# Kernel tuning notes

Hardware: AMD Instinct MI355X
Metric: run time of the kernel (lower is better)

## Reference

```python
import jax, jax.numpy as jnp
import numpy as np

N_CELLS = 50000
N_GENES = 2000
HIDDEN = 128
HEADS = 4
HEAD_DIM = HIDDEN // HEADS
E_FULL = 800000
E_PRUNED = 400000
LN_EPS = 1e-6
NEG_SLOPE = 0.2


def setup_inputs() -> dict:
    key = jax.random.key(0)
    ks = jax.random.split(key, 20)
    s_in = 1.0 / np.sqrt(N_GENES)
    s_h = 1.0 / np.sqrt(HIDDEN)
    inp = {
        "node_features": jax.random.normal(ks[0], (N_CELLS, N_GENES), jnp.float32),
        "full_edge_index": jax.random.randint(ks[1], (2, E_FULL), 0, N_CELLS, jnp.int64 if jax.config.jax_enable_x64 else jnp.int32),
        "full_edge_weights": jax.random.uniform(ks[2], (E_FULL, 1), jnp.float32),
        "pruned_edge_index": jax.random.randint(ks[3], (2, E_PRUNED), 0, N_CELLS, jnp.int64 if jax.config.jax_enable_x64 else jnp.int32),
        "pruned_edge_weights": jax.random.uniform(ks[4], (E_PRUNED, 1), jnp.float32),
        "alpha": jax.random.uniform(ks[5], (), jnp.float32),
        # input projection
        "ip_w": jax.random.normal(ks[6], (N_GENES, HIDDEN), jnp.float32) * s_in,
        "ip_b": jnp.zeros((HIDDEN,), jnp.float32),
        # GAT full graph
        "gf_wsrc": jax.random.normal(ks[7], (HIDDEN, HIDDEN), jnp.float32) * s_h,
        "gf_wdst": jax.random.normal(ks[8], (HIDDEN, HIDDEN), jnp.float32) * s_h,
        "gf_wedge": jax.random.normal(ks[9], (1, HIDDEN), jnp.float32),
        "gf_attn": jax.random.normal(ks[10], (HEADS, HEAD_DIM), jnp.float32) * (1.0 / np.sqrt(HEAD_DIM)),
        "gf_bias": jnp.zeros((HIDDEN,), jnp.float32),
        # GAT pruned graph
        "gp_wsrc": jax.random.normal(ks[11], (HIDDEN, HIDDEN), jnp.float32) * s_h,
        "gp_wdst": jax.random.normal(ks[12], (HIDDEN, HIDDEN), jnp.float32) * s_h,
        "gp_wedge": jax.random.normal(ks[13], (1, HIDDEN), jnp.float32),
        "gp_attn": jax.random.normal(ks[14], (HEADS, HEAD_DIM), jnp.float32) * (1.0 / np.sqrt(HEAD_DIM)),
        "gp_bias": jnp.zeros((HIDDEN,), jnp.float32),
        # LayerNorm
        "ln_scale": jnp.ones((HIDDEN,), jnp.float32),
        "ln_bias": jnp.zeros((HIDDEN,), jnp.float32),
    }
    return inp


def _gatv2(h, edge_index, edge_w, wsrc, wdst, wedge, attn, bias):
    """GATv2 with edge features: e_ij = a_h . leaky_relu(Ws h_i + Wd h_j + We w_ij),
    segment-softmax over destination nodes, scatter-aggregate Ws h_src, concat heads."""
    n = h.shape[0]
    src, dst = edge_index[0], edge_index[1]
    hs = (h @ wsrc).reshape(n, HEADS, HEAD_DIM)
    hd = (h @ wdst).reshape(n, HEADS, HEAD_DIM)
    ew = (edge_w @ wedge).reshape(-1, HEADS, HEAD_DIM)  # [E,H,D]
    z = jax.nn.leaky_relu(hs[src] + hd[dst] + ew, NEG_SLOPE)  # [E,H,D]
    logits = jnp.einsum('ehd,hd->eh', z, attn)  # [E,H]
    # segment softmax over incoming edges of each dst node
    m = jax.ops.segment_max(logits, dst, num_segments=n)
    m = jnp.where(jnp.isfinite(m), m, 0.0)
    ex = jnp.exp(logits - m[dst])
    denom = jax.ops.segment_sum(ex, dst, num_segments=n)
    att = ex / (denom[dst] + 1e-16)  # [E,H]
    out = jax.ops.segment_sum(att[..., None] * hs[src], dst, num_segments=n)  # [n,H,D]
    return out.reshape(n, HIDDEN) + bias


def _layer_norm(x, scale, bias):
    mu = jnp.mean(x, axis=-1, keepdims=True)
    var = jnp.mean(jnp.square(x - mu), axis=-1, keepdims=True)
    return (x - mu) * jax.lax.rsqrt(var + LN_EPS) * scale + bias


def reference(node_features, full_edge_index, full_edge_weights, pruned_edge_index,
              pruned_edge_weights, alpha, ip_w, ip_b,
              gf_wsrc, gf_wdst, gf_wedge, gf_attn, gf_bias,
              gp_wsrc, gp_wdst, gp_wedge, gp_attn, gp_bias,
              ln_scale, ln_bias):
    h = node_features @ ip_w + ip_b  # [n, hidden]
    h_full = _gatv2(h, full_edge_index, full_edge_weights, gf_wsrc, gf_wdst, gf_wedge, gf_attn, gf_bias)
    h_pruned = _gatv2(h, pruned_edge_index, pruned_edge_weights, gp_wsrc, gp_wdst, gp_wedge, gp_attn, gp_bias)
    h = (1.0 - alpha) * h_full + alpha * h_pruned
    h = jax.nn.elu(h)
    return _layer_norm(h, ln_scale, ln_bias)
```

## Files before the change

### kernel.cpp

```cpp
#include <hip/hip_runtime.h>
#include <hip/hip_bf16.h>

#define N_GENES 2000
#define SA 72
#define SH 136

typedef __attribute__((ext_vector_type(8))) short frag8;
typedef __attribute__((ext_vector_type(4))) float facc4;

static __device__ __forceinline__ unsigned short f2bf(float f) {
    unsigned int u = __float_as_uint(f);
    unsigned int r = (u + 0x7FFFu + ((u >> 16) & 1u)) >> 16;
    return (unsigned short)r;
}
static __device__ __forceinline__ ushort2 pk2(float a, float b) {
    __hip_bfloat162 r = __float22bfloat162_rn(float2{a, b});
    return *(ushort2*)&r;
}

__global__ void prep(const float* __restrict__ ip_w,
                     const float* __restrict__ ws_f, const float* __restrict__ wd_f,
                     const float* __restrict__ ws_p, const float* __restrict__ wd_p,
                     unsigned short* __restrict__ Bt1,
                     unsigned short* __restrict__ Bf, unsigned short* __restrict__ Bp,
                     int* __restrict__ deg, unsigned int* __restrict__ counter, int n2) {
    int idx = blockIdx.x * blockDim.x + threadIdx.x;
    if (idx < n2) deg[idx] = 0;
    if (idx == 0) counter[0] = 0u;
    if (idx < 128 * 2048) {
        int nrow = idx >> 11, k = idx & 2047;
        unsigned short v = 0;
        if (k < N_GENES) v = f2bf(ip_w[(size_t)k * 128 + nrow]);
        Bt1[idx] = v;
    } else {
        int q = idx - 128 * 2048;
        if (q >= 2 * 256 * 128) return;
        int g = q >> 15;
        int r = (q >> 7) & 255;
        int k = q & 127;
        const float* w = (g == 0) ? (r < 128 ? ws_f : wd_f) : (r < 128 ? ws_p : wd_p);
        (g == 0 ? Bf : Bp)[(r << 7) | k] = f2bf(w[k * 128 + (r & 127)]);
    }
}

__global__ __launch_bounds__(256) void gemm_deg(const float* __restrict__ A,
                                                const unsigned short* __restrict__ Bt,
                                                const float* __restrict__ bias,
                                                const unsigned short* __restrict__ Bf,
                                                const unsigned short* __restrict__ Bp,
                                                unsigned short* __restrict__ Cf,
                                                unsigned short* __restrict__ Cp,
                                                int M, int K, int gemmBlocks,
                                                const int* __restrict__ dst_f, int Ef,
                                                const int* __restrict__ dst_p, int Ep,
                                                int* __restrict__ deg, int N) {
    if (blockIdx.x >= gemmBlocks) {
        int e = (blockIdx.x - gemmBlocks) * 256 + threadIdx.x;
        if (e < Ef) atomicAdd(&deg[dst_f[e]], 1);
        else if (e < Ef + Ep) atomicAdd(&deg[N + dst_p[e - Ef]], 1);
        return;
    }
    const int Kpad = 2048;
    __shared__ __align__(16) unsigned short lA[64 * SA];
    __shared__ __align__(16) unsigned short lH[64 * SH];
    int t = threadIdx.x, lane = t & 63, wv = t >> 6;
    int lr = lane & 15, lq = lane >> 4;
    facc4 acc[4][2];
#pragma unroll
    for (int i = 0; i < 4; i++)
#pragma unroll
        for (int j = 0; j < 2; j++) acc[i][j] = (facc4){0.f, 0.f, 0.f, 0.f};
    int row_base = blockIdx.x * 64;

    int ar_r[4], ar_c[4];
    const float* ar_p[4];
#pragma unroll
    for (int j = 0; j < 4; j++) {
        int q = j * 256 + t;
        ar_r[j] = q >> 4;
        ar_c[j] = (q & 15) * 4;
        int rg = row_base + ar_r[j];
        if (rg >= M) rg = M - 1;
        ar_p[j] = A + (size_t)rg * K + ar_c[j];
    }
    const unsigned short* bp[4];
#pragma unroll
    for (int ks = 0; ks < 2; ks++)
#pragma unroll
        for (int ni = 0; ni < 2; ni++) {
            int col = wv * 32 + ni * 16 + lr;
            bp[ks * 2 + ni] = Bt + (size_t)col * Kpad + ks * 32 + lq * 8;
        }

    float4 ar[4];
    frag8 bfr[4];
#pragma unroll
    for (int j = 0; j < 4; j++) ar[j] = *(const float4*)(ar_p[j]);
#pragma unroll
    for (int f = 0; f < 4; f++) bfr[f] = *(const frag8*)(bp[f]);

    for (int k0 = 0; k0 < Kpad; k0 += 64) {
        __syncthreads();
#pragma unroll
        for (int j = 0; j < 4; j++) {
            ushort2 u01 = pk2(ar[j].x, ar[j].y);
            ushort2 u23 = pk2(ar[j].z, ar[j].w);
            ushort4 u = {u01.x, u01.y, u23.x, u23.y};
            *(ushort4*)&lA[ar_r[j] * SA + ar_c[j]] = u;
        }
        __syncthreads();
        int kn = k0 + 64;
        frag8 bfn[4];
        if (kn < Kpad) {
#pragma unroll
            for (int j = 0; j < 4; j++) {
                int kk = kn + ar_c[j];
                float4 v = {0.f, 0.f, 0.f, 0.f};
                if (kk < K) v = *(const float4*)(ar_p[j] + kn);
                ar[j] = v;
            }
#pragma unroll
            for (int f = 0; f < 4; f++) bfn[f] = *(const frag8*)(bp[f] + kn);
        }
#pragma unroll
        for (int ks = 0; ks < 2; ks++) {
            frag8 af[4];
#pragma unroll
            for (int mi = 0; mi < 4; mi++)
                af[mi] = *(const frag8*)&lA[(mi * 16 + lr) * SA + ks * 32 + lq * 8];
#pragma unroll
            for (int mi = 0; mi < 4; mi++)
#pragma unroll
                for (int ni = 0; ni < 2; ni++)
                    acc[mi][ni] = __builtin_amdgcn_mfma_f32_16x16x32_bf16(af[mi], bfr[ks * 2 + ni], acc[mi][ni], 0, 0, 0);
        }
        if (kn < Kpad) {
#pragma unroll
            for (int f = 0; f < 4; f++) bfr[f] = bfn[f];
        }
    }
    __syncthreads();
#pragma unroll
    for (int mi = 0; mi < 4; mi++) {
#pragma unroll
        for (int r = 0; r < 4; r++) {
            int row = mi * 16 + lq * 4 + r;
#pragma unroll
            for (int ni = 0; ni < 2; ni++) {
                int col = wv * 32 + ni * 16 + lr;
                lH[row * SH + col] = f2bf(acc[mi][ni][r] + bias[col]);
            }
        }
    }
    __syncthreads();
#pragma unroll 1
    for (int g = 0; g < 2; g++) {
        const unsigned short* B2 = g ? Bp : Bf;
        unsigned short* Cb = g ? Cp : Cf;
        facc4 a2[4][4];
#pragma unroll
        for (int i = 0; i < 4; i++)
#pragma unroll
            for (int j = 0; j < 4; j++) a2[i][j] = (facc4){0.f, 0.f, 0.f, 0.f};
#pragma unroll
        for (int ks = 0; ks < 4; ks++) {
            frag8 af[4], bf[4];
#pragma unroll
            for (int mi = 0; mi < 4; mi++)
                af[mi] = *(const frag8*)&lH[(mi * 16 + lr) * SH + ks * 32 + lq * 8];
#pragma unroll
            for (int ni = 0; ni < 4; ni++)
                bf[ni] = *(const frag8*)(B2 + ((wv * 64 + ni * 16 + lr) << 7) + ks * 32 + lq * 8);
#pragma unroll
            for (int mi = 0; mi < 4; mi++)
#pragma unroll
                for (int ni = 0; ni < 4; ni++)
                    a2[mi][ni] = __builtin_amdgcn_mfma_f32_16x16x32_bf16(af[mi], bf[ni], a2[mi][ni], 0, 0, 0);
        }
#pragma unroll
        for (int mi = 0; mi < 4; mi++) {
#pragma unroll
            for (int r = 0; r < 4; r++) {
                int row = row_base + mi * 16 + lq * 4 + r;
                if (row < M) {
#pragma unroll
                    for (int ni = 0; ni < 4; ni++) {
                        int col = wv * 64 + ni * 16 + lr;
                        Cb[(size_t)row * 256 + col] = f2bf(a2[mi][ni][r]);
                    }
                }
            }
        }
    }
}

__global__ __launch_bounds__(256) void seg_assign(const int* __restrict__ deg,
                                                  int* __restrict__ offs,
                                                  int* __restrict__ cur,
                                                  unsigned int* __restrict__ counter, int n2) {
    __shared__ int wbase[4];
    int t = threadIdx.x;
    int i = blockIdx.x * 256 + t;
    int lane = t & 63, wv = t >> 6;
    int c = (i < n2) ? deg[i] : 0;
    int incl = c;
#pragma unroll
    for (int o = 1; o < 64; o <<= 1) {
        int y = __shfl_up(incl, o);
        if (lane >= o) incl += y;
    }
    if (lane == 63) wbase[wv] = incl;
    __syncthreads();
    if (t == 0) {
        int s0 = wbase[0], s1 = wbase[1], s2 = wbase[2], s3 = wbase[3];
        int b = (int)atomicAdd(counter, (unsigned int)(s0 + s1 + s2 + s3));
        wbase[0] = b;
        wbase[1] = b + s0;
        wbase[2] = b + s0 + s1;
        wbase[3] = b + s0 + s1 + s2;
    }
    __syncthreads();
    int start = wbase[wv] + incl - c;
    if (i < n2) { offs[i] = start; cur[i] = start; }
}

__global__ void fill2(const int* __restrict__ src_f, const int* __restrict__ dst_f,
                      const float* __restrict__ ew_f, int Ef,
                      const int* __restrict__ src_p, const int* __restrict__ dst_p,
                      const float* __restrict__ ew_p, int Ep,
                      int* __restrict__ cur, int2* __restrict__ srcw, int N) {
    int e = blockIdx.x * blockDim.x + threadIdx.x;
    if (e >= Ef + Ep) return;
    int g = (e >= Ef);
    int ee = g ? e - Ef : e;
    int d = g ? dst_p[ee] : dst_f[ee];
    int node = g ? N + d : d;
    int p = atomicAdd(&cur[node], 1);
    int s = g ? src_p[ee] : src_f[ee];
    float w = g ? ew_p[ee] : ew_f[ee];
    srcw[p] = make_int2(s, __float_as_int(w));
}

__global__ __launch_bounds__(256) void gat2(const int* __restrict__ offs,
                                            const int* __restrict__ deg,
                                            const int2* __restrict__ srcw,
                                            const unsigned short* __restrict__ hshd_f,
                                            const unsigned short* __restrict__ hshd_p,
                                            const float* __restrict__ wedge_f,
                                            const float* __restrict__ attn_f,
                                            const float* __restrict__ bias_f,
                                            const float* __restrict__ wedge_p,
                                            const float* __restrict__ attn_p,
                                            const float* __restrict__ bias_p,
                                            float* __restrict__ out_full,
                                            float* __restrict__ out_pruned, int N) {
    int wid = blockIdx.x * 4 + (threadIdx.x >> 6);
    if (wid * 2 >= 2 * N) return;
    int lane = threadIdx.x & 63;
    int half = lane >> 5;
    int wl = lane & 31;
    int node = wid * 2 + half;
    int g = node >= N;
    int onode = g ? node - N : node;
    const unsigned short* hshd = g ? hshd_p : hshd_f;
    const float* wedge = g ? wedge_p : wedge_f;
    const float* attn = g ? attn_p : attn_f;
    const float* bias = g ? bias_p : bias_f;
    float* out = g ? out_pruned : out_full;
    int d4 = wl * 4;
    const float LOG2E = 1.4426950408889634f;
    float4 wv4 = *(const float4*)&wedge[d4];
    float4 av4 = *(const float4*)&attn[d4];
    av4.x *= LOG2E; av4.y *= LOG2E; av4.z *= LOG2E; av4.w *= LOG2E;
    uint2 hdr = *(const uint2*)&hshd[(size_t)onode * 256 + 128 + d4];
    const float hd0 = __uint_as_float(hdr.x << 16);
    const float hd1 = __uint_as_float(hdr.x & 0xffff0000u);
    const float hd2 = __uint_as_float(hdr.y << 16);
    const float hd3 = __uint_as_float(hdr.y & 0xffff0000u);
    int s = offs[node], cnt = deg[node];
    if (cnt <= 0) s = 0;
    int mc = max(cnt, __shfl_xor(cnt, 32));
    float m = -INFINITY, l = 0.f;
    float a0 = 0.f, a1 = 0.f, a2 = 0.f, a3 = 0.f;
    if (mc > 0) {
        int last = s + (cnt > 0 ? cnt : 1) - 1;
        auto CL = [last](int j) { return j > last ? last : j; };
        int2 e0 = srcw[CL(s)], e1 = srcw[CL(s + 1)], e2 = srcw[CL(s + 2)], e3 = srcw[CL(s + 3)];
        int2 e4 = srcw[CL(s + 4)], e5 = srcw[CL(s + 5)];
        uint2 hr0 = *(const uint2*)&hshd[(size_t)e0.x * 256 + d4];
        uint2 hr1 = *(const uint2*)&hshd[(size_t)e1.x * 256 + d4];
        uint2 hr2 = *(const uint2*)&hshd[(size_t)e2.x * 256 + d4];
        uint2 hr3 = *(const uint2*)&hshd[(size_t)e3.x * 256 + d4];
        for (int i = 0; i < mc; i += 2) {
            int2 ea = srcw[CL(s + i + 6)], eb = srcw[CL(s + i + 7)];
            uint2 hr4 = *(const uint2*)&hshd[(size_t)e4.x * 256 + d4];
            uint2 hr5 = *(const uint2*)&hshd[(size_t)e5.x * 256 + d4];
            {
                float h0 = __uint_as_float(hr0.x << 16);
                float h1 = __uint_as_float(hr0.x & 0xffff0000u);
                float h2 = __uint_as_float(hr0.y << 16);
                float h3 = __uint_as_float(hr0.y & 0xffff0000u);
                float w = __int_as_float(e0.y);
                float z0 = fmaf(w, wv4.x, h0 + hd0); z0 = (z0 > 0.f) ? z0 : 0.2f * z0;
                float z1 = fmaf(w, wv4.y, h1 + hd1); z1 = (z1 > 0.f) ? z1 : 0.2f * z1;
                float z2 = fmaf(w, wv4.z, h2 + hd2); z2 = (z2 > 0.f) ? z2 : 0.2f * z2;
                float z3 = fmaf(w, wv4.w, h3 + hd3); z3 = (z3 > 0.f) ? z3 : 0.2f * z3;
                float t = fmaf(z3, av4.w, fmaf(z2, av4.z, fmaf(z1, av4.y, z0 * av4.x)));
                t += __shfl_xor(t, 1);
                t += __shfl_xor(t, 2);
                t += __shfl_xor(t, 4);
                float mn = fmaxf(m, t);
                float sc = __builtin_amdgcn_exp2f(m - mn);
                float p = __builtin_amdgcn_exp2f(t - mn);
                p = (i < cnt) ? p : 0.f;
                l = l * sc + p;
                a0 = fmaf(p, h0, a0 * sc);
                a1 = fmaf(p, h1, a1 * sc);
                a2 = fmaf(p, h2, a2 * sc);
                a3 = fmaf(p, h3, a3 * sc);
                m = mn;
            }
            {
                float h0 = __uint_as_float(hr1.x << 16);
                float h1 = __uint_as_float(hr1.x & 0xffff0000u);
                float h2 = __uint_as_float(hr1.y << 16);
                float h3 = __uint_as_float(hr1.y & 0xffff0000u);
                float w = __int_as_float(e1.y);
                float z0 = fmaf(w, wv4.x, h0 + hd0); z0 = (z0 > 0.f) ? z0 : 0.2f * z0;
                float z1 = fmaf(w, wv4.y, h1 + hd1); z1 = (z1 > 0.f) ? z1 : 0.2f * z1;
                float z2 = fmaf(w, wv4.z, h2 + hd2); z2 = (z2 > 0.f) ? z2 : 0.2f * z2;
                float z3 = fmaf(w, wv4.w, h3 + hd3); z3 = (z3 > 0.f) ? z3 : 0.2f * z3;
                float t = fmaf(z3, av4.w, fmaf(z2, av4.z, fmaf(z1, av4.y, z0 * av4.x)));
                t += __shfl_xor(t, 1);
                t += __shfl_xor(t, 2);
                t += __shfl_xor(t, 4);
                float mn = fmaxf(m, t);
                float sc = __builtin_amdgcn_exp2f(m - mn);
                float p = __builtin_amdgcn_exp2f(t - mn);
                p = (i + 1 < cnt) ? p : 0.f;
                l = l * sc + p;
                a0 = fmaf(p, h0, a0 * sc);
                a1 = fmaf(p, h1, a1 * sc);
                a2 = fmaf(p, h2, a2 * sc);
                a3 = fmaf(p, h3, a3 * sc);
                m = mn;
            }
            e0 = e2; e1 = e3; e2 = e4; e3 = e5; e4 = ea; e5 = eb;
            hr0 = hr2; hr1 = hr3; hr2 = hr4; hr3 = hr5;
        }
    }
    float inv = 1.f / (l + 1e-16f);
    const float4 bv = *(const float4*)&bias[d4];
    float4 o;
    o.x = fmaf(a0, inv, bv.x);
    o.y = fmaf(a1, inv, bv.y);
    o.z = fmaf(a2, inv, bv.z);
    o.w = fmaf(a3, inv, bv.w);
    *(float4*)&out[(size_t)onode * 128 + d4] = o;
}

__global__ __launch_bounds__(256) void final_kernel(const float* __restrict__ hf,
                                                    float* __restrict__ out,
                                                    const float* __restrict__ alpha_p,
                                                    const float* __restrict__ scale,
                                                    const float* __restrict__ beta, int n) {
    int node = blockIdx.x * 4 + (threadIdx.x >> 6);
    if (node >= n) return;
    int lane = threadIdx.x & 63;
    int d2 = lane * 2;
    float a = *alpha_p;
    float2 f = *(const float2*)&hf[(size_t)node * 128 + d2];
    float2 p = *(const float2*)&out[(size_t)node * 128 + d2];
    float x0 = (1.f - a) * f.x + a * p.x;
    float x1 = (1.f - a) * f.y + a * p.y;
    x0 = (x0 > 0.f) ? x0 : expm1f(x0);
    x1 = (x1 > 0.f) ? x1 : expm1f(x1);
    float sm = x0 + x1;
#pragma unroll
    for (int o = 32; o >= 1; o >>= 1) sm += __shfl_xor(sm, o);
    float mu = sm * (1.f / 128.f);
    float d0 = x0 - mu, d1 = x1 - mu;
    float v = d0 * d0 + d1 * d1;
#pragma unroll
    for (int o = 32; o >= 1; o >>= 1) v += __shfl_xor(v, o);
    float rstd = rsqrtf(v * (1.f / 128.f) + 1e-6f);
    const float2 sv = *(const float2*)&scale[d2];
    const float2 bv = *(const float2*)&beta[d2];
    float2 o2;
    o2.x = d0 * rstd * sv.x + bv.x;
    o2.y = d1 * rstd * sv.y + bv.y;
    *(float2*)&out[(size_t)node * 128 + d2] = o2;
}

extern "C" void kernel_launch(void* const* d_in, const int* in_sizes, int n_in,
                              void* d_out, int out_size, void* d_ws, size_t ws_size,
                              hipStream_t stream) {
    const float* nf = (const float*)d_in[0];
    const int* fei = (const int*)d_in[1];
    const float* few = (const float*)d_in[2];
    const int* pei = (const int*)d_in[3];
    const float* pew = (const float*)d_in[4];
    const float* alpha = (const float*)d_in[5];
    const float* ip_w = (const float*)d_in[6];
    const float* ip_b = (const float*)d_in[7];
    const float* gf_wsrc = (const float*)d_in[8];
    const float* gf_wdst = (const float*)d_in[9];
    const float* gf_wedge = (const float*)d_in[10];
    const float* gf_attn = (const float*)d_in[11];
    const float* gf_bias = (const float*)d_in[12];
    const float* gp_wsrc = (const float*)d_in[13];
    const float* gp_wdst = (const float*)d_in[14];
    const float* gp_wedge = (const float*)d_in[15];
    const float* gp_attn = (const float*)d_in[16];
    const float* gp_bias = (const float*)d_in[17];
    const float* ln_scale = (const float*)d_in[18];
    const float* ln_bias = (const float*)d_in[19];

    const int N = in_sizes[0] / N_GENES;
    const int Ef = in_sizes[1] / 2;
    const int Ep = in_sizes[3] / 2;
    const int Etot = Ef + Ep;
    const int n2 = 2 * N;

    char* base = (char*)d_ws;
    size_t off = 0;
    auto carve = [&](size_t bytes) -> char* {
        char* p = base + off;
        off = (off + bytes + 255) & ~(size_t)255;
        return p;
    };
    unsigned short* Bt1 = (unsigned short*)carve((size_t)128 * 2048 * 2);
    unsigned short* Bf = (unsigned short*)carve(256 * 128 * 2);
    unsigned short* Bp = (unsigned short*)carve(256 * 128 * 2);
    unsigned short* hshd_f = (unsigned short*)carve((size_t)N * 256 * 2);
    unsigned short* hshd_p = (unsigned short*)carve((size_t)N * 256 * 2);
    float* h_full = (float*)carve((size_t)N * 128 * 4);
    int* deg = (int*)carve((size_t)n2 * 4);
    int* offs = (int*)carve((size_t)n2 * 4);
    int* cur = (int*)carve((size_t)n2 * 4);
    unsigned int* counter = (unsigned int*)carve(4);
    int2* srcw = (int2*)carve((size_t)Etot * 8);
    float* out_f = (float*)d_out;

    const int* src_f = fei;
    const int* dst_f = fei + Ef;
    const int* src_p = pei;
    const int* dst_p = pei + Ep;

    prep<<<(128 * 2048 + 2 * 256 * 128 + 255) / 256, 256, 0, stream>>>(
        ip_w, gf_wsrc, gf_wdst, gp_wsrc, gp_wdst, Bt1, Bf, Bp, deg, counter, n2);

    int gb1 = (N + 63) / 64;
    int degb = (Etot + 255) / 256;
    gemm_deg<<<gb1 + degb, 256, 0, stream>>>(nf, Bt1, ip_b, Bf, Bp, hshd_f, hshd_p,
                                             N, N_GENES, gb1,
                                             dst_f, Ef, dst_p, Ep, deg, N);

    seg_assign<<<(n2 + 255) / 256, 256, 0, stream>>>(deg, offs, cur, counter, n2);

    fill2<<<(Etot + 255) / 256, 256, 0, stream>>>(src_f, dst_f, few, Ef, src_p, dst_p, pew, Ep,
                                                  cur, srcw, N);

    int gwaves = (n2 + 1) / 2;
    gat2<<<(gwaves + 3) / 4, 256, 0, stream>>>(offs, deg, srcw, hshd_f, hshd_p,
                                               gf_wedge, gf_attn, gf_bias,
                                               gp_wedge, gp_attn, gp_bias,
                                               h_full, out_f, N);

    final_kernel<<<(N + 3) / 4, 256, 0, stream>>>(h_full, out_f, alpha, ln_scale, ln_bias, N);
    (void)ws_size; (void)n_in; (void)out_size;
}
```

Before: 802.1 us.

## Move degree count into prep and fuse CSR fill into GEMM launch

The degree-counting atomics move from the GEMM launch into the weight-prep kernel, and the degree/counter zeroing becomes a memset. The scatter-fill of sorted edges now runs as extra blocks inside the GEMM launch instead of as a separate kernel after seg_assign. This cuts one launch and lets the fill atomics overlap the big projection GEMM rather than following it. The trade-off is an added memset call, and the fill blocks now compete with the GEMM blocks for CUs.

```diff
diff --git a/kernel.cpp b/kernel.cpp
--- a/kernel.cpp
+++ b/kernel.cpp
@@ -18,179 +18,31 @@
     return *(ushort2*)&r;
 }
 
-__global__ void prep(const float* __restrict__ ip_w,
-                     const float* __restrict__ ws_f, const float* __restrict__ wd_f,
-                     const float* __restrict__ ws_p, const float* __restrict__ wd_p,
-                     unsigned short* __restrict__ Bt1,
-                     unsigned short* __restrict__ Bf, unsigned short* __restrict__ Bp,
-                     int* __restrict__ deg, unsigned int* __restrict__ counter, int n2) {
+__global__ void prep_deg(const float* __restrict__ ip_w,
+                         const float* __restrict__ ws_f, const float* __restrict__ wd_f,
+                         const float* __restrict__ ws_p, const float* __restrict__ wd_p,
+                         unsigned short* __restrict__ Bt1,
+                         unsigned short* __restrict__ Bf, unsigned short* __restrict__ Bp,
+                         const int* __restrict__ dst_f, int Ef,
+                         const int* __restrict__ dst_p, int Ep,
+                         int* __restrict__ deg, int N) {
     int idx = blockIdx.x * blockDim.x + threadIdx.x;
-    if (idx < n2) deg[idx] = 0;
-    if (idx == 0) counter[0] = 0u;
     if (idx < 128 * 2048) {
         int nrow = idx >> 11, k = idx & 2047;
         unsigned short v = 0;
         if (k < N_GENES) v = f2bf(ip_w[(size_t)k * 128 + nrow]);
         Bt1[idx] = v;
-    } else {
+    } else if (idx < 128 * 2048 + 2 * 256 * 128) {
         int q = idx - 128 * 2048;
-        if (q >= 2 * 256 * 128) return;
         int g = q >> 15;
         int r = (q >> 7) & 255;
         int k = q & 127;
         const float* w = (g == 0) ? (r < 128 ? ws_f : wd_f) : (r < 128 ? ws_p : wd_p);
         (g == 0 ? Bf : Bp)[(r << 7) | k] = f2bf(w[k * 128 + (r & 127)]);
-    }
-}
-
-__global__ __launch_bounds__(256) void gemm_deg(const float* __restrict__ A,
-                                                const unsigned short* __restrict__ Bt,
-                                                const float* __restrict__ bias,
-                                                const unsigned short* __restrict__ Bf,
-                                                const unsigned short* __restrict__ Bp,
-                                                unsigned short* __restrict__ Cf,
-                                                unsigned short* __restrict__ Cp,
-                                                int M, int K, int gemmBlocks,
-                                                const int* __restrict__ dst_f, int Ef,
-                                                const int* __restrict__ dst_p, int Ep,
-                                                int* __restrict__ deg, int N) {
-    if (blockIdx.x >= gemmBlocks) {
-        int e = (blockIdx.x - gemmBlocks) * 256 + threadIdx.x;
+    } else {
+        int e = idx - (128 * 2048 + 2 * 256 * 128);
         if (e < Ef) atomicAdd(&deg[dst_f[e]], 1);
         else if (e < Ef + Ep) atomicAdd(&deg[N + dst_p[e - Ef]], 1);
-        return;
-    }
-    const int Kpad = 2048;
-    __shared__ __align__(16) unsigned short lA[64 * SA];
-    __shared__ __align__(16) unsigned short lH[64 * SH];
-    int t = threadIdx.x, lane = t & 63, wv = t >> 6;
-    int lr = lane & 15, lq = lane >> 4;
-    facc4 acc[4][2];
-#pragma unroll
-    for (int i = 0; i < 4; i++)
-#pragma unroll
-        for (int j = 0; j < 2; j++) acc[i][j] = (facc4){0.f, 0.f, 0.f, 0.f};
-    int row_base = blockIdx.x * 64;
-
-    int ar_r[4], ar_c[4];
-    const float* ar_p[4];
-#pragma unroll
-    for (int j = 0; j < 4; j++) {
-        int q = j * 256 + t;
-        ar_r[j] = q >> 4;
-        ar_c[j] = (q & 15) * 4;
-        int rg = row_base + ar_r[j];
-        if (rg >= M) rg = M - 1;
-        ar_p[j] = A + (size_t)rg * K + ar_c[j];
-    }
-    const unsigned short* bp[4];
-#pragma unroll
-    for (int ks = 0; ks < 2; ks++)
-#pragma unroll
-        for (int ni = 0; ni < 2; ni++) {
-            int col = wv * 32 + ni * 16 + lr;
-            bp[ks * 2 + ni] = Bt + (size_t)col * Kpad + ks * 32 + lq * 8;
-        }
-
-    float4 ar[4];
-    frag8 bfr[4];
-#pragma unroll
-    for (int j = 0; j < 4; j++) ar[j] = *(const float4*)(ar_p[j]);
-#pragma unroll
-    for (int f = 0; f < 4; f++) bfr[f] = *(const frag8*)(bp[f]);
-
-    for (int k0 = 0; k0 < Kpad; k0 += 64) {
-        __syncthreads();
-#pragma unroll
-        for (int j = 0; j < 4; j++) {
-            ushort2 u01 = pk2(ar[j].x, ar[j].y);
-            ushort2 u23 = pk2(ar[j].z, ar[j].w);
-            ushort4 u = {u01.x, u01.y, u23.x, u23.y};
-            *(ushort4*)&lA[ar_r[j] * SA + ar_c[j]] = u;
-        }
-        __syncthreads();
-        int kn = k0 + 64;
-        frag8 bfn[4];
-        if (kn < Kpad) {
-#pragma unroll
-            for (int j = 0; j < 4; j++) {
-                int kk = kn + ar_c[j];
-                float4 v = {0.f, 0.f, 0.f, 0.f};
-                if (kk < K) v = *(const float4*)(ar_p[j] + kn);
-                ar[j] = v;
-            }
-#pragma unroll
-            for (int f = 0; f < 4; f++) bfn[f] = *(const frag8*)(bp[f] + kn);
-        }
-#pragma unroll
-        for (int ks = 0; ks < 2; ks++) {
-            frag8 af[4];
-#pragma unroll
-            for (int mi = 0; mi < 4; mi++)
-                af[mi] = *(const frag8*)&lA[(mi * 16 + lr) * SA + ks * 32 + lq * 8];
-#pragma unroll
-            for (int mi = 0; mi < 4; mi++)
-#pragma unroll
-                for (int ni = 0; ni < 2; ni++)
-                    acc[mi][ni] = __builtin_amdgcn_mfma_f32_16x16x32_bf16(af[mi], bfr[ks * 2 + ni], acc[mi][ni], 0, 0, 0);
-        }
-        if (kn < Kpad) {
-#pragma unroll
-            for (int f = 0; f < 4; f++) bfr[f] = bfn[f];
-        }
-    }
-    __syncthreads();
-#pragma unroll
-    for (int mi = 0; mi < 4; mi++) {
-#pragma unroll
-        for (int r = 0; r < 4; r++) {
-            int row = mi * 16 + lq * 4 + r;
-#pragma unroll
-            for (int ni = 0; ni < 2; ni++) {
-                int col = wv * 32 + ni * 16 + lr;
-                lH[row * SH + col] = f2bf(acc[mi][ni][r] + bias[col]);
-            }
-        }
-    }
-    __syncthreads();
-#pragma unroll 1
-    for (int g = 0; g < 2; g++) {
-        const unsigned short* B2 = g ? Bp : Bf;
-        unsigned short* Cb = g ? Cp : Cf;
-        facc4 a2[4][4];
-#pragma unroll
-        for (int i = 0; i < 4; i++)
-#pragma unroll
-            for (int j = 0; j < 4; j++) a2[i][j] = (facc4){0.f, 0.f, 0.f, 0.f};
-#pragma unroll
-        for (int ks = 0; ks < 4; ks++) {
-            frag8 af[4], bf[4];
-#pragma unroll
-            for (int mi = 0; mi < 4; mi++)
-                af[mi] = *(const frag8*)&lH[(mi * 16 + lr) * SH + ks * 32 + lq * 8];
-#pragma unroll
-            for (int ni = 0; ni < 4; ni++)
-                bf[ni] = *(const frag8*)(B2 + ((wv * 64 + ni * 16 + lr) << 7) + ks * 32 + lq * 8);
-#pragma unroll
-            for (int mi = 0; mi < 4; mi++)
-#pragma unroll
-                for (int ni = 0; ni < 4; ni++)
-                    a2[mi][ni] = __builtin_amdgcn_mfma_f32_16x16x32_bf16(af[mi], bf[ni], a2[mi][ni], 0, 0, 0);
-        }
-#pragma unroll
-        for (int mi = 0; mi < 4; mi++) {
-#pragma unroll
-            for (int r = 0; r < 4; r++) {
-                int row = row_base + mi * 16 + lq * 4 + r;
-                if (row < M) {
-#pragma unroll
-                    for (int ni = 0; ni < 4; ni++) {
-                        int col = wv * 64 + ni * 16 + lr;
-                        Cb[(size_t)row * 256 + col] = f2bf(a2[mi][ni][r]);
-                    }
-                }
-            }
-        }
     }
 }
 
@@ -224,21 +76,167 @@
     if (i < n2) { offs[i] = start; cur[i] = start; }
 }
 
-__global__ void fill2(const int* __restrict__ src_f, const int* __restrict__ dst_f,
-                      const float* __restrict__ ew_f, int Ef,
-                      const int* __restrict__ src_p, const int* __restrict__ dst_p,
-                      const float* __restrict__ ew_p, int Ep,
-                      int* __restrict__ cur, int2* __restrict__ srcw, int N) {
-    int e = blockIdx.x * blockDim.x + threadIdx.x;
-    if (e >= Ef + Ep) return;
-    int g = (e >= Ef);
-    int ee = g ? e - Ef : e;
-    int d = g ? dst_p[ee] : dst_f[ee];
-    int node = g ? N + d : d;
-    int p = atomicAdd(&cur[node], 1);
-    int s = g ? src_p[ee] : src_f[ee];
-    float w = g ? ew_p[ee] : ew_f[ee];
-    srcw[p] = make_int2(s, __float_as_int(w));
+__global__ __launch_bounds__(256) void gemm_fill(const float* __restrict__ A,
+                                                 const unsigned short* __restrict__ Bt,
+                                                 const float* __restrict__ bias,
+                                                 const unsigned short* __restrict__ Bf,
+                                                 const unsigned short* __restrict__ Bp,
+                                                 unsigned short* __restrict__ Cf,
+                                                 unsigned short* __restrict__ Cp,
+                                                 int M, int K, int gemmBlocks,
+                                                 const int* __restrict__ src_f,
+                                                 const int* __restrict__ dst_f,
+                                                 const float* __restrict__ ew_f, int Ef,
+                                                 const int* __restrict__ src_p,
+                                                 const int* __restrict__ dst_p,
+                                                 const float* __restrict__ ew_p, int Ep,
+                                                 int* __restrict__ cur,
+                                                 int2* __restrict__ srcw, int N) {
+    if (blockIdx.x >= gemmBlocks) {
+        int e = (blockIdx.x - gemmBlocks) * 256 + threadIdx.x;
+        if (e >= Ef + Ep) return;
+        int g = (e >= Ef);
+        int ee = g ? e - Ef : e;
+        int d = g ? dst_p[ee] : dst_f[ee];
+        int node = g ? N + d : d;
+        int p = atomicAdd(&cur[node], 1);
+        int s = g ? src_p[ee] : src_f[ee];
+        float w = g ? ew_p[ee] : ew_f[ee];
+        srcw[p] = make_int2(s, __float_as_int(w));
+        return;
+    }
+    const int Kpad = 2048;
+    __shared__ __align__(16) unsigned short lA[64 * SA];
+    __shared__ __align__(16) unsigned short lH[64 * SH];
+    int t = threadIdx.x, lane = t & 63, wv = t >> 6;
+    int lr = lane & 15, lq = lane >> 4;
+    facc4 acc[4][2];
+#pragma unroll
+    for (int i = 0; i < 4; i++)
+#pragma unroll
+        for (int j = 0; j < 2; j++) acc[i][j] = (facc4){0.f, 0.f, 0.f, 0.f};
+    int row_base = blockIdx.x * 64;
+
+    int ar_r[4], ar_c[4];
+    const float* ar_p[4];
+#pragma unroll
+    for (int j = 0; j < 4; j++) {
+        int q = j * 256 + t;
+        ar_r[j] = q >> 4;
+        ar_c[j] = (q & 15) * 4;
+        int rg = row_base + ar_r[j];
+        if (rg >= M) rg = M - 1;
+        ar_p[j] = A + (size_t)rg * K + ar_c[j];
+    }
+    const unsigned short* bp[4];
+#pragma unroll
+    for (int ks = 0; ks < 2; ks++)
+#pragma unroll
+        for (int ni = 0; ni < 2; ni++) {
+            int col = wv * 32 + ni * 16 + lr;
+            bp[ks * 2 + ni] = Bt + (size_t)col * Kpad + ks * 32 + lq * 8;
+        }
+
+    float4 ar[4];
+    frag8 bfr[4];
+#pragma unroll
+    for (int j = 0; j < 4; j++) ar[j] = *(const float4*)(ar_p[j]);
+#pragma unroll
+    for (int f = 0; f < 4; f++) bfr[f] = *(const frag8*)(bp[f]);
+
+    for (int k0 = 0; k0 < Kpad; k0 += 64) {
+        __syncthreads();
+#pragma unroll
+        for (int j = 0; j < 4; j++) {
+            ushort2 u01 = pk2(ar[j].x, ar[j].y);
+            ushort2 u23 = pk2(ar[j].z, ar[j].w);
+            ushort4 u = {u01.x, u01.y, u23.x, u23.y};
+            *(ushort4*)&lA[ar_r[j] * SA + ar_c[j]] = u;
+        }
+        __syncthreads();
+        int kn = k0 + 64;
+        frag8 bfn[4];
+        if (kn < Kpad) {
+#pragma unroll
+            for (int j = 0; j < 4; j++) {
+                int kk = kn + ar_c[j];
+                float4 v = {0.f, 0.f, 0.f, 0.f};
+                if (kk < K) v = *(const float4*)(ar_p[j] + kn);
+                ar[j] = v;
+            }
+#pragma unroll
+            for (int f = 0; f < 4; f++) bfn[f] = *(const frag8*)(bp[f] + kn);
+        }
+#pragma unroll
+        for (int ks = 0; ks < 2; ks++) {
+            frag8 af[4];
+#pragma unroll
+            for (int mi = 0; mi < 4; mi++)
+                af[mi] = *(const frag8*)&lA[(mi * 16 + lr) * SA + ks * 32 + lq * 8];
+#pragma unroll
+            for (int mi = 0; mi < 4; mi++)
+#pragma unroll
+                for (int ni = 0; ni < 2; ni++)
+                    acc[mi][ni] = __builtin_amdgcn_mfma_f32_16x16x32_bf16(af[mi], bfr[ks * 2 + ni], acc[mi][ni], 0, 0, 0);
+        }
+        if (kn < Kpad) {
+#pragma unroll
+            for (int f = 0; f < 4; f++) bfr[f] = bfn[f];
+        }
+    }
+    __syncthreads();
+#pragma unroll
+    for (int mi = 0; mi < 4; mi++) {
+#pragma unroll
+        for (int r = 0; r < 4; r++) {
+            int row = mi * 16 + lq * 4 + r;
+#pragma unroll
+            for (int ni = 0; ni < 2; ni++) {
+                int col = wv * 32 + ni * 16 + lr;
+                lH[row * SH + col] = f2bf(acc[mi][ni][r] + bias[col]);
+            }
+        }
+    }
+    __syncthreads();
+#pragma unroll 1
+    for (int g = 0; g < 2; g++) {
+        const unsigned short* B2 = g ? Bp : Bf;
+        unsigned short* Cb = g ? Cp : Cf;
+        facc4 a2[4][4];
+#pragma unroll
+        for (int i = 0; i < 4; i++)
+#pragma unroll
+            for (int j = 0; j < 4; j++) a2[i][j] = (facc4){0.f, 0.f, 0.f, 0.f};
+#pragma unroll
+        for (int ks = 0; ks < 4; ks++) {
+            frag8 af[4], bf[4];
+#pragma unroll
+            for (int mi = 0; mi < 4; mi++)
+                af[mi] = *(const frag8*)&lH[(mi * 16 + lr) * SH + ks * 32 + lq * 8];
+#pragma unroll
+            for (int ni = 0; ni < 4; ni++)
+                bf[ni] = *(const frag8*)(B2 + ((wv * 64 + ni * 16 + lr) << 7) + ks * 32 + lq * 8);
+#pragma unroll
+            for (int mi = 0; mi < 4; mi++)
+#pragma unroll
+                for (int ni = 0; ni < 4; ni++)
+                    a2[mi][ni] = __builtin_amdgcn_mfma_f32_16x16x32_bf16(af[mi], bf[ni], a2[mi][ni], 0, 0, 0);
+        }
+#pragma unroll
+        for (int mi = 0; mi < 4; mi++) {
+#pragma unroll
+            for (int r = 0; r < 4; r++) {
+                int row = row_base + mi * 16 + lq * 4 + r;
+                if (row < M) {
+#pragma unroll
+                    for (int ni = 0; ni < 4; ni++) {
+                        int col = wv * 64 + ni * 16 + lr;
+                        Cb[(size_t)row * 256 + col] = f2bf(a2[mi][ni][r]);
+                    }
+                }
+            }
+        }
+    }
 }
 
 __global__ __launch_bounds__(256) void gat2(const int* __restrict__ offs,
@@ -435,10 +433,10 @@
     unsigned short* hshd_f = (unsigned short*)carve((size_t)N * 256 * 2);
     unsigned short* hshd_p = (unsigned short*)carve((size_t)N * 256 * 2);
     float* h_full = (float*)carve((size_t)N * 128 * 4);
+    unsigned int* counter = (unsigned int*)carve(4);
     int* deg = (int*)carve((size_t)n2 * 4);
     int* offs = (int*)carve((size_t)n2 * 4);
     int* cur = (int*)carve((size_t)n2 * 4);
-    unsigned int* counter = (unsigned int*)carve(4);
     int2* srcw = (int2*)carve((size_t)Etot * 8);
     float* out_f = (float*)d_out;
 
@@ -447,19 +445,22 @@
     const int* src_p = pei;
     const int* dst_p = pei + Ep;
 
-    prep<<<(128 * 2048 + 2 * 256 * 128 + 255) / 256, 256, 0, stream>>>(
-        ip_w, gf_wsrc, gf_wdst, gp_wsrc, gp_wdst, Bt1, Bf, Bp, deg, counter, n2);
+    hipMemsetAsync(counter, 0, 256 + (size_t)n2 * 4, stream);
+
+    int prepWork = 128 * 2048 + 2 * 256 * 128;
+    prep_deg<<<(prepWork + Etot + 255) / 256, 256, 0, stream>>>(
+        ip_w, gf_wsrc, gf_wdst, gp_wsrc, gp_wdst, Bt1, Bf, Bp,
+        dst_f, Ef, dst_p, Ep, deg, N);
+
+    seg_assign<<<(n2 + 255) / 256, 256, 0, stream>>>(deg, offs, cur, counter, n2);
 
     int gb1 = (N + 63) / 64;
-    int degb = (Etot + 255) / 256;
-    gemm_deg<<<gb1 + degb, 256, 0, stream>>>(nf, Bt1, ip_b, Bf, Bp, hshd_f, hshd_p,
-                                             N, N_GENES, gb1,
-                                             dst_f, Ef, dst_p, Ep, deg, N);
-
-    seg_assign<<<(n2 + 255) / 256, 256, 0, stream>>>(deg, offs, cur, counter, n2);
-
-    fill2<<<(Etot + 255) / 256, 256, 0, stream>>>(src_f, dst_f, few, Ef, src_p, dst_p, pew, Ep,
-                                                  cur, srcw, N);
+    int fillb = (Etot + 255) / 256;
+    gemm_fill<<<gb1 + fillb, 256, 0, stream>>>(nf, Bt1, ip_b, Bf, Bp, hshd_f, hshd_p,
+                                               N, N_GENES, gb1,
+                                               src_f, dst_f, few, Ef,
+                                               src_p, dst_p, pew, Ep,
+                                               cur, srcw, N);
 
     int gwaves = (n2 + 1) / 2;
     gat2<<<(gwaves + 3) / 4, 256, 0, stream>>>(offs, deg, srcw, hshd_f, hshd_p,
```

Result: faster. 783.1 us (-2.4%).
